# Kernel optimization log

Measured on AMD Instinct MI355X. Metric: run time of the kernel, lower is better.

Reference implementation:

```python
import jax, jax.numpy as jnp
import numpy as np
from jax import lax

ALPHA = 2.0
EROSIONS = 10


def setup_inputs() -> dict:
    key = jax.random.key(0)
    k1, k2 = jax.random.split(key)
    B, C, H, W = 32, 1, 1024, 1024
    pred = jax.random.uniform(k1, (B, C, H, W), dtype=jnp.float32)
    target = jax.random.uniform(k2, (B, C, H, W), dtype=jnp.float32)
    return {"pred": pred, "target": target}


def _hausdorff_er_loss(pred, target):
    # 3x3 cross structuring element * 0.2 (sums to 1), as in kernel2D
    kernel = jnp.array([[0.0, 0.2, 0.0],
                        [0.2, 0.2, 0.2],
                        [0.0, 0.2, 0.0]], dtype=pred.dtype)
    kernel = kernel[None, None]  # OIHW: (1,1,3,3)

    bound = (pred - target) ** 2  # (B,1,H,W)

    def step(carry, k):
        b, acc = carry
        # scipy.ndimage.convolve(mode='constant', cval=0) == SAME zero-padded conv;
        # the cross kernel is symmetric so correlation == convolution.
        dil = lax.conv_general_dilated(
            b, kernel, window_strides=(1, 1), padding='SAME',
            dimension_numbers=('NCHW', 'OIHW', 'NCHW'))
        er = jnp.maximum(dil - 0.5, 0.0)
        # per-sample min/max normalization (ptp over the whole (1,H,W) array)
        emin = er.min(axis=(1, 2, 3), keepdims=True)
        emax = er.max(axis=(1, 2, 3), keepdims=True)
        ptp = emax - emin
        er = jnp.where(ptp > 0, (er - emin) / jnp.where(ptp > 0, ptp, 1.0), er)
        acc = acc + er * (k + 1.0) ** ALPHA
        return (er, acc), None

    ks = jnp.arange(EROSIONS, dtype=bound.dtype)
    (_, eroted), _ = lax.scan(step, (bound, jnp.zeros_like(bound)), ks)
    return eroted.mean()


def reference(pred, target):
    return _hausdorff_er_loss(pred, target)
```

## Files before the change

kernel.cpp:

```cpp
#include <hip/hip_runtime.h>

#define BATCH 32
#define HH 1024
#define WW 1024
#define NPIX (HH * WW)
#define NEROS 10
#define TPS 64
#define NTILES (BATCH * TPS)

__device__ __forceinline__ float4 ld4f(const float* p) {
    return *reinterpret_cast<const float4*>(p);
}

template <bool FIRST>
__global__ __launch_bounds__(256, 4) void conv_er_kernel(
    const float* __restrict__ pred, const float* __restrict__ tgt,
    const float* __restrict__ in, float* __restrict__ out,
    const unsigned short* __restrict__ Fprev, unsigned short* __restrict__ Fout,
    const unsigned* __restrict__ cntPrev, unsigned* __restrict__ cntOut,
    const unsigned* __restrict__ pmin, const unsigned* __restrict__ pmax,
    unsigned* __restrict__ omin, unsigned* __restrict__ omax,
    double* __restrict__ osum) {
    if (!FIRST && *cntPrev == 0u) return;

    int blk = blockIdx.x;
    blk = (blk & 7) * (NTILES >> 3) + (blk >> 3);
    const int s = blk >> 6, ty = blk & 63, ry = ty << 4;
    const int tid = threadIdx.x, lane = tid & 63, w = tid >> 6;
    const int xb = lane << 4;
    const size_t sbase = (size_t)s * NPIX;

    unsigned M = 0x3FFFFu;
    if (!FIRST) {
        const unsigned short* Fs = Fprev + s * TPS;
        M = ((unsigned)Fs[ty]) << 1;
        if (ty > 0) M |= (Fs[ty - 1] >> 15) & 1u;
        if (ty < TPS - 1) M |= ((unsigned)(Fs[ty + 1] & 1u)) << 17;
        if (M == 0u) {
            if (tid == 0) {
                Fout[s * TPS + ty] = 0;
                atomicMin(&omin[s], 0u);
            }
            return;
        }
    }

    float a = 1.f, cc = 0.f;
    if (!FIRST) {
        const float mn = __uint_as_float(pmin[s]);
        const float mx = __uint_as_float(pmax[s]);
        const float ptp = mx - mn;
        if (ptp > 0.f) { a = 1.f / ptp; cc = mn; }
    }

    const int r0 = w << 2;

    float A[16], B[16], C[16], O[16];

    auto loadRow = [&](int y, float* V) {
        bool ok = (y >= 0 && y < HH);
        if (!FIRST) ok = ok && (((M >> (y - ry + 1)) & 1u) != 0u);
        if (!ok) {
#pragma unroll
            for (int j = 0; j < 16; ++j) V[j] = 0.f;
            return;
        }
        const size_t idx = sbase + (size_t)y * WW + xb;
#pragma unroll
        for (int q = 0; q < 4; ++q) {
            if constexpr (FIRST) {
                const float4 p = ld4f(pred + idx + 4 * q);
                const float4 t = ld4f(tgt + idx + 4 * q);
                V[4 * q + 0] = (p.x - t.x) * (p.x - t.x);
                V[4 * q + 1] = (p.y - t.y) * (p.y - t.y);
                V[4 * q + 2] = (p.z - t.z) * (p.z - t.z);
                V[4 * q + 3] = (p.w - t.w) * (p.w - t.w);
            } else {
                const float4 v = ld4f(in + idx + 4 * q);
                V[4 * q + 0] = v.x;
                V[4 * q + 1] = v.y;
                V[4 * q + 2] = v.z;
                V[4 * q + 3] = v.w;
            }
        }
    };

    loadRow(ry + r0 - 1, A);
    loadRow(ry + r0, B);

    float lmin = 3.4e38f, lmax = 0.f, lsum = 0.f;
    unsigned rowbits = 0u;

#pragma unroll
    for (int r = 0; r < 4; ++r) {
        const int y = ry + r0 + r;
        loadRow(y + 1, C);
        const bool act = FIRST || (((M >> (r0 + r)) & 7u) != 0u);
        if (act) {
            float lfe = __shfl_up(B[15], 1);
            if (lane == 0) lfe = 0.f;
            float rte = __shfl_down(B[0], 1);
            if (lane == 63) rte = 0.f;
            const float vert =
                1.f + (y > 0 ? 1.f : 0.f) + (y < HH - 1 ? 1.f : 0.f);
            bool nz = false;
#pragma unroll
            for (int j = 0; j < 16; ++j) {
                const float lf = (j == 0) ? lfe : B[j - 1];
                const float rt = (j == 15) ? rte : B[j + 1];
                const float conv = 0.2f * (A[j] + C[j] + B[j] + lf + rt);
                float dil;
                if constexpr (FIRST) {
                    dil = conv;
                } else {
                    const int x = xb + j;
                    const float kf =
                        0.2f * (vert + (x > 0 ? 1.f : 0.f) +
                                (x < WW - 1 ? 1.f : 0.f));
                    dil = (conv - cc * kf) * a;
                }
                const float er = fmaxf(dil - 0.5f, 0.f);
                O[j] = er;
                lmin = fminf(lmin, er);
                lmax = fmaxf(lmax, er);
                lsum += er;
                nz = nz || (er > 0.f);
            }
            if (__ballot(nz) != 0ull) {
                const size_t oidx = sbase + (size_t)y * WW + xb;
#pragma unroll
                for (int q = 0; q < 4; ++q)
                    *reinterpret_cast<float4*>(out + oidx + 4 * q) =
                        make_float4(O[4 * q], O[4 * q + 1], O[4 * q + 2],
                                    O[4 * q + 3]);
                rowbits |= 1u << (r0 + r);
            }
        } else {
            lmin = fminf(lmin, 0.f);
        }
#pragma unroll
        for (int j = 0; j < 16; ++j) {
            A[j] = B[j];
            B[j] = C[j];
        }
    }

#pragma unroll
    for (int off = 32; off > 0; off >>= 1) {
        lmin = fminf(lmin, __shfl_down(lmin, off));
        lmax = fmaxf(lmax, __shfl_down(lmax, off));
        lsum += __shfl_down(lsum, off);
    }
    __shared__ float smn[4], smx[4], ssm[4];
    __shared__ unsigned sfb[4];
    if (lane == 0) {
        smn[w] = lmin;
        smx[w] = lmax;
        ssm[w] = lsum;
        sfb[w] = rowbits;
    }
    __syncthreads();
    if (tid == 0) {
        const unsigned fmask = sfb[0] | sfb[1] | sfb[2] | sfb[3];
        float bmn = smn[0], bmx = smx[0], bsm = ssm[0];
#pragma unroll
        for (int i = 1; i < 4; ++i) {
            bmn = fminf(bmn, smn[i]);
            bmx = fmaxf(bmx, smx[i]);
            bsm += ssm[i];
        }
        Fout[s * TPS + ty] = (unsigned short)fmask;
        if (fmask) atomicAdd(cntOut, 1u);
        atomicMin(&omin[s], __float_as_uint(bmn));
        if (bmx > 0.f) atomicMax(&omax[s], __float_as_uint(bmx));
        if (bsm > 0.f) atomicAdd(&osum[s], (double)bsm);
    }
}

__global__ void init_kernel(unsigned* __restrict__ minb,
                            unsigned* __restrict__ maxb,
                            double* __restrict__ sums,
                            unsigned* __restrict__ cnt) {
    const int i = blockIdx.x * blockDim.x + threadIdx.x;
    if (i < NEROS * BATCH) {
        minb[i] = 0x7f800000u;
        maxb[i] = 0u;
        sums[i] = 0.0;
    }
    if (i < NEROS) cnt[i] = 0u;
}

__global__ void final_kernel(const unsigned* __restrict__ minb,
                             const unsigned* __restrict__ maxb,
                             const double* __restrict__ sums,
                             float* __restrict__ out) {
    const int s = threadIdx.x;
    double tot = 0.0;
    if (s < BATCH) {
        for (int k = 0; k < NEROS; ++k) {
            const float mn = __uint_as_float(minb[k * BATCH + s]);
            const float mx = __uint_as_float(maxb[k * BATCH + s]);
            const double sm = sums[k * BATCH + s];
            const float ptp = mx - mn;
            double v;
            if (ptp > 0.f)
                v = (sm - (double)NPIX * (double)mn) / (double)ptp;
            else
                v = sm;
            tot += (double)((k + 1) * (k + 1)) * v;
        }
    }
#pragma unroll
    for (int off = 32; off > 0; off >>= 1) tot += __shfl_down(tot, off);
    if (s == 0) out[0] = (float)(tot / ((double)BATCH * (double)NPIX));
}

extern "C" void kernel_launch(void* const* d_in, const int* in_sizes, int n_in,
                              void* d_out, int out_size, void* d_ws,
                              size_t ws_size, hipStream_t stream) {
    const float* pred = (const float*)d_in[0];
    const float* tgt = (const float*)d_in[1];
    float* out = (float*)d_out;

    float* buf0 = (float*)d_ws;
    float* buf1 = buf0 + (size_t)BATCH * NPIX;
    unsigned* minb = (unsigned*)(buf1 + (size_t)BATCH * NPIX);
    unsigned* maxb = minb + NEROS * BATCH;
    double* sums = (double*)(maxb + NEROS * BATCH);
    unsigned short* F = (unsigned short*)(sums + NEROS * BATCH);
    unsigned* cnt = (unsigned*)(F + (size_t)NEROS * NTILES);

    init_kernel<<<2, 256, 0, stream>>>(minb, maxb, sums, cnt);

    dim3 grid(NTILES), block(256);
    conv_er_kernel<true><<<grid, block, 0, stream>>>(
        pred, tgt, nullptr, buf0, nullptr, F, nullptr, &cnt[0], nullptr,
        nullptr, minb, maxb, sums);

    float* bufs[2] = {buf0, buf1};
    for (int k = 1; k < NEROS; ++k) {
        const float* src = bufs[(k - 1) & 1];
        float* dst = bufs[k & 1];
        conv_er_kernel<false><<<grid, block, 0, stream>>>(
            nullptr, nullptr, src, dst, F + (size_t)(k - 1) * NTILES,
            F + (size_t)k * NTILES, &cnt[k - 1], &cnt[k],
            minb + (size_t)(k - 1) * BATCH, maxb + (size_t)(k - 1) * BATCH,
            minb + (size_t)k * BATCH, maxb + (size_t)k * BATCH,
            sums + (size_t)k * BATCH);
    }

    final_kernel<<<1, 64, 0, stream>>>(minb, maxb, sums, out);
}
```

Baseline: 147.3 us.

## Stage first erosion pass through LDS tile with coalesced loads and bitmask atomics

```diff
diff --git a/kernel.cpp b/kernel.cpp
--- a/kernel.cpp
+++ b/kernel.cpp
@@ -7,21 +7,144 @@
 #define NEROS 10
 #define TPS 64
 #define NTILES (BATCH * TPS)
+#define FWPS 32
 
 __device__ __forceinline__ float4 ld4f(const float* p) {
     return *reinterpret_cast<const float4*>(p);
 }
 
-template <bool FIRST>
-__global__ __launch_bounds__(256, 4) void conv_er_kernel(
+__global__ __launch_bounds__(512, 4) void conv0_kernel(
     const float* __restrict__ pred, const float* __restrict__ tgt,
+    float* __restrict__ out, unsigned* __restrict__ Fout,
+    unsigned* __restrict__ cntOut, unsigned* __restrict__ omin,
+    unsigned* __restrict__ omax, double* __restrict__ osum) {
+    int blk = blockIdx.x;
+    blk = (blk & 7) * (NTILES >> 3) + (blk >> 3);
+    const int s = blk >> 6, ty = blk & 63, ry = ty << 4;
+    const int tid = threadIdx.x, lane = tid & 63, w = tid >> 6;
+    const size_t sbase = (size_t)s * NPIX;
+
+    __shared__ float sb[18 * 1024];
+
+    float4 pv[9], tv[9];
+#pragma unroll
+    for (int i = 0; i < 9; ++i) {
+        const int slot = tid + 512 * i;
+        const int y = ry - 1 + (slot >> 8);
+        if (y >= 0 && y < HH) {
+            const size_t idx = sbase + (size_t)y * WW + ((slot & 255) << 2);
+            pv[i] = ld4f(pred + idx);
+            tv[i] = ld4f(tgt + idx);
+        } else {
+            pv[i] = make_float4(0.f, 0.f, 0.f, 0.f);
+            tv[i] = make_float4(0.f, 0.f, 0.f, 0.f);
+        }
+    }
+#pragma unroll
+    for (int i = 0; i < 9; ++i) {
+        const int slot = tid + 512 * i;
+        float4 b;
+        b.x = (pv[i].x - tv[i].x) * (pv[i].x - tv[i].x);
+        b.y = (pv[i].y - tv[i].y) * (pv[i].y - tv[i].y);
+        b.z = (pv[i].z - tv[i].z) * (pv[i].z - tv[i].z);
+        b.w = (pv[i].w - tv[i].w) * (pv[i].w - tv[i].w);
+        *reinterpret_cast<float4*>(
+            &sb[(slot >> 8) * 1024 + ((slot & 255) << 2)]) = b;
+    }
+    __syncthreads();
+
+    float lmin = 3.4e38f, lmax = 0.f, lsum = 0.f;
+    unsigned rowbits = 0u;
+#pragma unroll
+    for (int rr = 0; rr < 2; ++rr) {
+        const int yl = (w << 1) + rr;
+        const int y = ry + yl;
+        float O[16];
+        bool nz = false;
+#pragma unroll
+        for (int q = 0; q < 4; ++q) {
+            const int xw = (q << 8) + (lane << 2);
+            const float4 U = *(const float4*)&sb[yl * 1024 + xw];
+            const float4 Cc = *(const float4*)&sb[(yl + 1) * 1024 + xw];
+            const float4 D = *(const float4*)&sb[(yl + 2) * 1024 + xw];
+            float lf = __shfl_up(Cc.w, 1);
+            if (lane == 0)
+                lf = (q > 0) ? sb[(yl + 1) * 1024 + (q << 8) - 1] : 0.f;
+            float rt = __shfl_down(Cc.x, 1);
+            if (lane == 63)
+                rt = (q < 3) ? sb[(yl + 1) * 1024 + (q << 8) + 256] : 0.f;
+            const float cv[4] = {Cc.x, Cc.y, Cc.z, Cc.w};
+            const float uv[4] = {U.x, U.y, U.z, U.w};
+            const float dv[4] = {D.x, D.y, D.z, D.w};
+            const float lvv[4] = {lf, Cc.x, Cc.y, Cc.z};
+            const float rvv[4] = {Cc.y, Cc.z, Cc.w, rt};
+#pragma unroll
+            for (int j = 0; j < 4; ++j) {
+                const float conv =
+                    0.2f * (uv[j] + dv[j] + cv[j] + lvv[j] + rvv[j]);
+                const float er = fmaxf(conv - 0.5f, 0.f);
+                O[(q << 2) + j] = er;
+                lmin = fminf(lmin, er);
+                lmax = fmaxf(lmax, er);
+                lsum += er;
+                nz = nz || (er > 0.f);
+            }
+        }
+        if (__ballot(nz) != 0ull) {
+            const size_t ob = sbase + (size_t)y * WW;
+#pragma unroll
+            for (int q = 0; q < 4; ++q)
+                *reinterpret_cast<float4*>(out + ob + (q << 8) + (lane << 2)) =
+                    make_float4(O[q << 2], O[(q << 2) + 1], O[(q << 2) + 2],
+                                O[(q << 2) + 3]);
+            rowbits |= 1u << yl;
+        }
+    }
+
+#pragma unroll
+    for (int off = 32; off > 0; off >>= 1) {
+        lmin = fminf(lmin, __shfl_down(lmin, off));
+        lmax = fmaxf(lmax, __shfl_down(lmax, off));
+        lsum += __shfl_down(lsum, off);
+    }
+    __shared__ float smn[8], smx[8], ssm[8];
+    __shared__ unsigned sfb[8];
+    if (lane == 0) {
+        smn[w] = lmin;
+        smx[w] = lmax;
+        ssm[w] = lsum;
+        sfb[w] = rowbits;
+    }
+    __syncthreads();
+    if (tid == 0) {
+        unsigned fmask = 0u;
+        float bmn = smn[0], bmx = smx[0], bsm = ssm[0];
+        fmask = sfb[0];
+#pragma unroll
+        for (int i = 1; i < 8; ++i) {
+            bmn = fminf(bmn, smn[i]);
+            bmx = fmaxf(bmx, smx[i]);
+            bsm += ssm[i];
+            fmask |= sfb[i];
+        }
+        if (fmask) {
+            atomicOr(&Fout[s * FWPS + (ty >> 1)], fmask << ((ty & 1) * 16));
+            atomicAdd(cntOut, 1u);
+        }
+        atomicMin(&omin[s], __float_as_uint(bmn));
+        if (bmx > 0.f) atomicMax(&omax[s], __float_as_uint(bmx));
+        if (bsm > 0.f) atomicAdd(&osum[s], (double)bsm);
+    }
+}
+
+__global__ __launch_bounds__(256, 4) void convt_kernel(
     const float* __restrict__ in, float* __restrict__ out,
-    const unsigned short* __restrict__ Fprev, unsigned short* __restrict__ Fout,
+    const unsigned* __restrict__ Fprev, unsigned* __restrict__ Fout,
     const unsigned* __restrict__ cntPrev, unsigned* __restrict__ cntOut,
     const unsigned* __restrict__ pmin, const unsigned* __restrict__ pmax,
     unsigned* __restrict__ omin, unsigned* __restrict__ omax,
     double* __restrict__ osum) {
-    if (!FIRST && *cntPrev == 0u) return;
+    if (*cntPrev == 0u) return;
 
     int blk = blockIdx.x;
     blk = (blk & 7) * (NTILES >> 3) + (blk >> 3);
@@ -30,23 +153,23 @@
     const int xb = lane << 4;
     const size_t sbase = (size_t)s * NPIX;
 
-    unsigned M = 0x3FFFFu;
-    if (!FIRST) {
-        const unsigned short* Fs = Fprev + s * TPS;
-        M = ((unsigned)Fs[ty]) << 1;
-        if (ty > 0) M |= (Fs[ty - 1] >> 15) & 1u;
-        if (ty < TPS - 1) M |= ((unsigned)(Fs[ty + 1] & 1u)) << 17;
-        if (M == 0u) {
-            if (tid == 0) {
-                Fout[s * TPS + ty] = 0;
-                atomicMin(&omin[s], 0u);
-            }
-            return;
-        }
+    const unsigned* Fs = Fprev + s * FWPS;
+    const int w32 = ty >> 1, sh = (ty & 1) * 16;
+    const unsigned cur = Fs[w32];
+    unsigned M = ((cur >> sh) & 0xFFFFu) << 1;
+    if (ty > 0)
+        M |= (ty & 1) ? ((cur >> 15) & 1u) : ((Fs[w32 - 1] >> 31) & 1u);
+    if (ty < TPS - 1) {
+        const unsigned nb = (ty & 1) ? (Fs[w32 + 1] & 1u) : ((cur >> 16) & 1u);
+        M |= nb << 17;
+    }
+    if (M == 0u) {
+        if (tid == 0) atomicMin(&omin[s], 0u);
+        return;
     }
 
     float a = 1.f, cc = 0.f;
-    if (!FIRST) {
+    {
         const float mn = __uint_as_float(pmin[s]);
         const float mx = __uint_as_float(pmax[s]);
         const float ptp = mx - mn;
@@ -54,12 +177,11 @@
     }
 
     const int r0 = w << 2;
-
     float A[16], B[16], C[16], O[16];
 
     auto loadRow = [&](int y, float* V) {
-        bool ok = (y >= 0 && y < HH);
-        if (!FIRST) ok = ok && (((M >> (y - ry + 1)) & 1u) != 0u);
+        const bool ok =
+            (y >= 0 && y < HH) && (((M >> (y - ry + 1)) & 1u) != 0u);
         if (!ok) {
 #pragma unroll
             for (int j = 0; j < 16; ++j) V[j] = 0.f;
@@ -68,20 +190,11 @@
         const size_t idx = sbase + (size_t)y * WW + xb;
 #pragma unroll
         for (int q = 0; q < 4; ++q) {
-            if constexpr (FIRST) {
-                const float4 p = ld4f(pred + idx + 4 * q);
-                const float4 t = ld4f(tgt + idx + 4 * q);
-                V[4 * q + 0] = (p.x - t.x) * (p.x - t.x);
-                V[4 * q + 1] = (p.y - t.y) * (p.y - t.y);
-                V[4 * q + 2] = (p.z - t.z) * (p.z - t.z);
-                V[4 * q + 3] = (p.w - t.w) * (p.w - t.w);
-            } else {
-                const float4 v = ld4f(in + idx + 4 * q);
-                V[4 * q + 0] = v.x;
-                V[4 * q + 1] = v.y;
-                V[4 * q + 2] = v.z;
-                V[4 * q + 3] = v.w;
-            }
+            const float4 v = ld4f(in + idx + 4 * q);
+            V[4 * q + 0] = v.x;
+            V[4 * q + 1] = v.y;
+            V[4 * q + 2] = v.z;
+            V[4 * q + 3] = v.w;
         }
     };
 
@@ -95,7 +208,7 @@
     for (int r = 0; r < 4; ++r) {
         const int y = ry + r0 + r;
         loadRow(y + 1, C);
-        const bool act = FIRST || (((M >> (r0 + r)) & 7u) != 0u);
+        const bool act = (((M >> (r0 + r)) & 7u) != 0u);
         if (act) {
             float lfe = __shfl_up(B[15], 1);
             if (lane == 0) lfe = 0.f;
@@ -109,16 +222,10 @@
                 const float lf = (j == 0) ? lfe : B[j - 1];
                 const float rt = (j == 15) ? rte : B[j + 1];
                 const float conv = 0.2f * (A[j] + C[j] + B[j] + lf + rt);
-                float dil;
-                if constexpr (FIRST) {
-                    dil = conv;
-                } else {
-                    const int x = xb + j;
-                    const float kf =
-                        0.2f * (vert + (x > 0 ? 1.f : 0.f) +
-                                (x < WW - 1 ? 1.f : 0.f));
-                    dil = (conv - cc * kf) * a;
-                }
+                const int x = xb + j;
+                const float kf = 0.2f * (vert + (x > 0 ? 1.f : 0.f) +
+                                         (x < WW - 1 ? 1.f : 0.f));
+                const float dil = (conv - cc * kf) * a;
                 const float er = fmaxf(dil - 0.5f, 0.f);
                 O[j] = er;
                 lmin = fminf(lmin, er);
@@ -169,8 +276,10 @@
             bmx = fmaxf(bmx, smx[i]);
             bsm += ssm[i];
         }
-        Fout[s * TPS + ty] = (unsigned short)fmask;
-        if (fmask) atomicAdd(cntOut, 1u);
+        if (fmask) {
+            atomicOr(&Fout[s * FWPS + w32], fmask << sh);
+            atomicAdd(cntOut, 1u);
+        }
         atomicMin(&omin[s], __float_as_uint(bmn));
         if (bmx > 0.f) atomicMax(&omax[s], __float_as_uint(bmx));
         if (bsm > 0.f) atomicAdd(&osum[s], (double)bsm);
@@ -180,6 +289,7 @@
 __global__ void init_kernel(unsigned* __restrict__ minb,
                             unsigned* __restrict__ maxb,
                             double* __restrict__ sums,
+                            unsigned* __restrict__ F,
                             unsigned* __restrict__ cnt) {
     const int i = blockIdx.x * blockDim.x + threadIdx.x;
     if (i < NEROS * BATCH) {
@@ -187,6 +297,7 @@
         maxb[i] = 0u;
         sums[i] = 0.0;
     }
+    if (i < NEROS * BATCH * FWPS) F[i] = 0u;
     if (i < NEROS) cnt[i] = 0u;
 }
 
@@ -227,23 +338,21 @@
     unsigned* minb = (unsigned*)(buf1 + (size_t)BATCH * NPIX);
     unsigned* maxb = minb + NEROS * BATCH;
     double* sums = (double*)(maxb + NEROS * BATCH);
-    unsigned short* F = (unsigned short*)(sums + NEROS * BATCH);
-    unsigned* cnt = (unsigned*)(F + (size_t)NEROS * NTILES);
-
-    init_kernel<<<2, 256, 0, stream>>>(minb, maxb, sums, cnt);
-
-    dim3 grid(NTILES), block(256);
-    conv_er_kernel<true><<<grid, block, 0, stream>>>(
-        pred, tgt, nullptr, buf0, nullptr, F, nullptr, &cnt[0], nullptr,
-        nullptr, minb, maxb, sums);
+    unsigned* F = (unsigned*)(sums + NEROS * BATCH);
+    unsigned* cnt = F + (size_t)NEROS * BATCH * FWPS;
+
+    init_kernel<<<40, 256, 0, stream>>>(minb, maxb, sums, F, cnt);
+
+    conv0_kernel<<<NTILES, 512, 0, stream>>>(pred, tgt, buf0, F, &cnt[0], minb,
+                                             maxb, sums);
 
     float* bufs[2] = {buf0, buf1};
     for (int k = 1; k < NEROS; ++k) {
         const float* src = bufs[(k - 1) & 1];
         float* dst = bufs[k & 1];
-        conv_er_kernel<false><<<grid, block, 0, stream>>>(
-            nullptr, nullptr, src, dst, F + (size_t)(k - 1) * NTILES,
-            F + (size_t)k * NTILES, &cnt[k - 1], &cnt[k],
+        convt_kernel<<<NTILES, 256, 0, stream>>>(
+            src, dst, F + (size_t)(k - 1) * BATCH * FWPS,
+            F + (size_t)k * BATCH * FWPS, &cnt[k - 1], &cnt[k],
             minb + (size_t)(k - 1) * BATCH, maxb + (size_t)(k - 1) * BATCH,
             minb + (size_t)k * BATCH, maxb + (size_t)k * BATCH,
             sums + (size_t)k * BATCH);
```

Measured after the change: 131.3 us. 10.9% less time.
